# Performance work log

Measured on AMD Instinct MI355X. Metric: run time of the kernel, lower is better.

## Reference

```python
import jax, jax.numpy as jnp
import numpy as np

COS_EPS = 1e-8  # torch F.cosine_similarity eps


def setup_inputs() -> dict:
    key = jax.random.key(0)
    k1, k2 = jax.random.split(key)
    x = jax.random.normal(k1, (8192, 512), dtype=jnp.float32)
    class_logits = jax.random.normal(k2, (8192, 100), dtype=jnp.float32)
    return {"x": x, "class_logits": class_logits}


def reference(x, class_logits):
    N, D = x.shape
    C = class_logits.shape[1]

    # class_logits.clone().detach()
    logits = jax.lax.stop_gradient(class_logits)
    pred = jax.nn.softmax(logits, axis=1)
    max_logit = pred.max(axis=1)          # [N]
    max_cls = pred.argmax(axis=1)         # [N] int

    # graph(): pairwise cosine similarity = normalize rows + gram matmul
    norms = jnp.linalg.norm(x, axis=1, keepdims=True)
    xn = x / jnp.maximum(norms, COS_EPS)
    mat = xn @ xn.T                       # [N, N]

    x_agg = mat @ x + x                   # [N, D]
    x_new = jax.lax.stop_gradient(x_agg)

    # update_prototype: per-class weighted scatter-add then mean over counts
    weighted = x_new * max_logit[:, None]                     # [N, D]
    sums = jax.ops.segment_sum(weighted, max_cls, num_segments=C)      # [C, D]
    counts = jax.ops.segment_sum(jnp.ones((N,), x.dtype), max_cls, num_segments=C)  # [C]
    prototypes = jnp.where(counts[:, None] > 0,
                           sums / jnp.maximum(counts, 1.0)[:, None],
                           jnp.zeros_like(sums))              # [C, D]

    # inter_class_matrix[i, j] = prototypes[j] - prototypes[i]
    inter_class_matrix = prototypes[None, :, :] - prototypes[:, None, :]  # [C, C, D]
    return prototypes, inter_class_matrix
```

## Files before the change

### kernel.cpp

```cpp
#include <hip/hip_runtime.h>
#include <math.h>

#define N_ROWS 8192
#define D_DIM  512
#define C_CLS  100

typedef unsigned short u16;
typedef unsigned int u32;
typedef __attribute__((ext_vector_type(8))) _Float16 half8;
typedef __attribute__((ext_vector_type(4))) float floatx4;

#define WS_G      0
#define WS_GP     262144
#define WS_INV    5505024
#define WS_WV     5513216
#define WS_CLS    5521408
#define WS_CNT    5529600
#define WS_OFFS   5529728
#define WS_ORDER  5529856
#define WS_U      5538048
#define WS_V      5589248
#define WS_ZTH    5640448

typedef const __attribute__((address_space(1))) u32* gp32;
typedef __attribute__((address_space(3))) u32* lp32;
__device__ __forceinline__ void cp16(const u16* g, u16* l) {
    __builtin_amdgcn_global_load_lds((gp32)g, (lp32)l, 16, 0, 0);
}

__device__ __forceinline__ u16 f2h(float v) {
    _Float16 h = (_Float16)v;
    return *(u16*)&h;
}

__global__ __launch_bounds__(256) void kA(const float* __restrict__ logits,
        const float* __restrict__ x, float* __restrict__ wv, int* __restrict__ cls,
        float* __restrict__ inv, u16* __restrict__ zth) {
    __shared__ float xs[32 * 516];
    __shared__ float ns[8][32];
    __shared__ float sv_s[32];
    int bx = blockIdx.x, t = threadIdx.x;
    if (bx < 1024) {
        int lane = t & 63;
        int row0 = (bx << 3) + ((t >> 6) << 1);
        #pragma unroll
        for (int rr = 0; rr < 2; ++rr) {
            int row = row0 + rr;
            const float* lrow = logits + (size_t)row * C_CLS;
            float v1 = lrow[lane];
            bool has2 = (lane + 64) < C_CLS;
            float v2 = has2 ? lrow[lane + 64] : -INFINITY;
            float m; int idx;
            if (v2 > v1) { m = v2; idx = lane + 64; } else { m = v1; idx = lane; }
            #pragma unroll
            for (int off = 32; off >= 1; off >>= 1) {
                float om = __shfl_down(m, off);
                int   oi = __shfl_down(idx, off);
                if (om > m || (om == m && oi < idx)) { m = om; idx = oi; }
            }
            m = __shfl(m, 0);
            idx = __shfl(idx, 0);
            float s = expf(v1 - m) + (has2 ? expf(v2 - m) : 0.0f);
            #pragma unroll
            for (int off = 32; off >= 1; off >>= 1) s += __shfl_down(s, off);
            if (lane == 0) {
                wv[row] = 1.0f / s;
                cls[row] = idx;
            }
        }
        return;
    }
    int r0 = (bx - 1024) << 5;
    const float* src = x + (size_t)r0 * D_DIM;
    #pragma unroll
    for (int i = 0; i < 16; ++i) {
        int e = i * 1024 + t * 4;
        int r = e >> 9, c = e & 511;
        *(float4*)&xs[r * 516 + c] = *(const float4*)&src[e];
    }
    __syncthreads();
    {
        int r = t & 31, seg = t >> 5;
        const float* row = &xs[r * 516 + seg * 64];
        float ss = 0.f;
        #pragma unroll
        for (int jj = 0; jj < 64; ++jj) { float v = row[jj]; ss += v * v; }
        ns[seg][r] = ss;
    }
    __syncthreads();
    if (t < 32) {
        float ss = ns[0][t] + ns[1][t] + ns[2][t] + ns[3][t]
                 + ns[4][t] + ns[5][t] + ns[6][t] + ns[7][t];
        float iv = 1.0f / fmaxf(sqrtf(ss), 1e-8f);
        inv[r0 + t] = iv;
        sv_s[t] = sqrtf(iv);
    }
    __syncthreads();
    int c = t >> 2, rq = (t & 3) * 8;
    float svl[8];
    #pragma unroll
    for (int ii = 0; ii < 8; ++ii) svl[ii] = sv_s[rq + ii];
    #pragma unroll
    for (int ct = 0; ct < 8; ++ct) {
        int d = ct * 64 + c;
        u16 o[8];
        #pragma unroll
        for (int ii = 0; ii < 8; ++ii)
            o[ii] = f2h(xs[(rq + ii) * 516 + d] * svl[ii]);
        uint4 val = make_uint4((u32)o[0] | ((u32)o[1] << 16),
                               (u32)o[2] | ((u32)o[3] << 16),
                               (u32)o[4] | ((u32)o[5] << 16),
                               (u32)o[6] | ((u32)o[7] << 16));
        *(uint4*)&zth[(size_t)d * N_ROWS + r0 + rq] = val;
    }
}

__global__ __launch_bounds__(1024) void kB(const int* __restrict__ cls,
        int* __restrict__ cnt, int* __restrict__ offs, int* __restrict__ order) {
    __shared__ int hist[128], scan_s[128], cur[128];
    int t = threadIdx.x;
    if (t < 128) hist[t] = 0;
    __syncthreads();
    for (int m = t; m < N_ROWS; m += 1024) atomicAdd(&hist[cls[m]], 1);
    __syncthreads();
    if (t < 128) scan_s[t] = hist[t];
    __syncthreads();
    #pragma unroll
    for (int d = 1; d < 128; d <<= 1) {
        int add = (t < 128 && t >= d) ? scan_s[t - d] : 0;
        __syncthreads();
        if (t < 128) scan_s[t] += add;
        __syncthreads();
    }
    if (t < 128) {
        int off0 = scan_s[t] - hist[t];
        cur[t] = off0;
        offs[t] = off0;
        cnt[t] = hist[t];
    }
    __syncthreads();
    for (int m = t; m < N_ROWS; m += 1024) {
        int p = atomicAdd(&cur[cls[m]], 1);
        order[p] = m;
    }
}

__global__ __launch_bounds__(256) void kC(const u16* __restrict__ zth,
        const float* __restrict__ x, const float* __restrict__ inv,
        const float* __restrict__ wv, const int* __restrict__ order,
        const int* __restrict__ offs, const int* __restrict__ cnt,
        float* __restrict__ Gp, float* __restrict__ u_arr, float* __restrict__ v_arr) {
    __shared__ __attribute__((aligned(16))) union {
        struct { u16 Ah[128 * 32], Bh[128 * 32]; } g;
        struct { float us[4][64], vs[4][64]; } uv;
    } sm;
    int bx = blockIdx.x, t = threadIdx.x;
    if (bx >= 320) {
        int idx = bx - 320;
        int c = idx >> 3, jc = idx & 7;
        int g = t >> 6, lane = t & 63;
        int j = jc * 64 + lane;
        int n = cnt[c], o = offs[c];
        float ua = 0.f, va = 0.f;
        for (int p = g; p < n; p += 4) {
            int m = order[o + p];
            float wm = wv[m];
            float wi = wm * inv[m];
            float xv = x[(size_t)m * D_DIM + j];
            ua += wi * xv; va += wm * xv;
        }
        sm.uv.us[g][lane] = ua; sm.uv.vs[g][lane] = va;
        __syncthreads();
        if (g == 0) {
            u_arr[(size_t)c * D_DIM + j] = sm.uv.us[0][lane] + sm.uv.us[1][lane] + sm.uv.us[2][lane] + sm.uv.us[3][lane];
            v_arr[(size_t)c * D_DIM + j] = sm.uv.vs[0][lane] + sm.uv.vs[1][lane] + sm.uv.vs[2][lane] + sm.uv.vs[3][lane];
        }
        return;
    }
    int tile = bx % 10;
    int p = bx / 10;
    int ti = tile < 4 ? 0 : (tile < 7 ? 1 : (tile < 9 ? 2 : 3));
    int tj = tile - (ti == 0 ? 0 : (ti == 1 ? 3 : (ti == 2 ? 5 : 6)));
    int i0 = ti << 7, j0 = tj << 7;
    bool diag = (ti == tj);
    int kb = p << 8;
    int w = t >> 6, l = t & 63;
    int srow = t >> 2, scol = (t & 3) << 3;
    int lm = l & 15, lg = l >> 4;
    floatx4 acc[4][4];
    #pragma unroll
    for (int mi = 0; mi < 4; ++mi)
        #pragma unroll
        for (int ni = 0; ni < 4; ++ni) acc[mi][ni] = (floatx4){0.f, 0.f, 0.f, 0.f};
    int d0 = srow * 32 + scol;
    int d1 = (64 + srow) * 32 + scol;
    const size_t ga0 = (size_t)(i0 + srow) * N_ROWS + kb + scol;
    const size_t ga1 = (size_t)(i0 + 64 + srow) * N_ROWS + kb + scol;
    const size_t gb0 = (size_t)(j0 + srow) * N_ROWS + kb + scol;
    const size_t gb1 = (size_t)(j0 + 64 + srow) * N_ROWS + kb + scol;
    const u16* Bhs = diag ? sm.g.Ah : sm.g.Bh;
    for (int s = 0; s < 8; ++s) {
        int ks = s << 5;
        cp16(zth + ga0 + ks, sm.g.Ah + d0);
        cp16(zth + ga1 + ks, sm.g.Ah + d1);
        if (!diag) {
            cp16(zth + gb0 + ks, sm.g.Bh + d0);
            cp16(zth + gb1 + ks, sm.g.Bh + d1);
        }
        __syncthreads();
        half8 ah[4], bh[4];
        #pragma unroll
        for (int mi = 0; mi < 4; ++mi) {
            int off = (((w & 1) << 6) + (mi << 4) + lm) * 32 + (lg << 3);
            ah[mi] = *(const half8*)&sm.g.Ah[off];
        }
        #pragma unroll
        for (int ni = 0; ni < 4; ++ni) {
            int off = (((w >> 1) << 6) + (ni << 4) + lm) * 32 + (lg << 3);
            bh[ni] = *(const half8*)&Bhs[off];
        }
        #pragma unroll
        for (int mi = 0; mi < 4; ++mi)
            #pragma unroll
            for (int ni = 0; ni < 4; ++ni)
                acc[mi][ni] = __builtin_amdgcn_mfma_f32_16x16x32_f16(ah[mi], bh[ni], acc[mi][ni], 0, 0, 0);
        __syncthreads();
    }
    float* Gb = Gp + ((size_t)(p * 10 + tile) << 14);
    #pragma unroll
    for (int mi = 0; mi < 4; ++mi) {
        int row0 = ((w & 1) << 6) + (mi << 4) + (lg << 2);
        #pragma unroll
        for (int ni = 0; ni < 4; ++ni) {
            int col = ((w >> 1) << 6) + (ni << 4) + lm;
            #pragma unroll
            for (int r = 0; r < 4; ++r)
                Gb[(size_t)(row0 + r) * 128 + col] = acc[mi][ni][r];
        }
    }
}

__global__ __launch_bounds__(256) void kR(const float* __restrict__ Gp,
                                          float* __restrict__ G) {
    int i = blockIdx.x * 256 + threadIdx.x;
    int r = i >> 9, c = i & 511;
    int tr = r >> 7, tc = c >> 7, rr = r & 127, cc = c & 127;
    if (tr > tc) { int tmp = tr; tr = tc; tc = tmp; tmp = rr; rr = cc; cc = tmp; }
    int tid = tr * 4 + tc - ((tr * (tr + 1)) >> 1);
    const float* src = Gp + ((size_t)tid << 14) + rr * 128 + cc;
    float s = 0.f;
    #pragma unroll
    for (int p = 0; p < 32; ++p) s += src[(size_t)p * 163840];
    G[i] = s;
}

__global__ __launch_bounds__(256) void kD(const float* __restrict__ u_arr,
        const float* __restrict__ v_arr, const int* __restrict__ cnt,
        const float* __restrict__ G, float* __restrict__ out) {
    __shared__ float us[8][512];
    int g = blockIdx.x >> 4;
    int panel = blockIdx.x & 15;
    int t = threadIdx.x;
    for (int idx = t; idx < 8 * 512; idx += 256) {
        int ci = idx >> 9, k = idx & 511;
        int cc = g * 8 + ci;
        us[ci][k] = (cc < C_CLS) ? u_arr[(size_t)cc * D_DIM + k] : 0.f;
    }
    __syncthreads();
    int ci = t >> 5, cj = t & 31;
    int c = g * 8 + ci;
    int j = panel * 32 + cj;
    float acc = 0.f;
    #pragma unroll 8
    for (int k = 0; k < D_DIM; ++k)
        acc += us[ci][k] * G[(size_t)k * D_DIM + j];
    if (c < C_CLS) {
        int n = cnt[c];
        float s = (n > 0) ? 1.0f / (float)n : 0.0f;
        out[(size_t)c * D_DIM + j] = (v_arr[(size_t)c * D_DIM + j] + acc) * s;
    }
}

__global__ __launch_bounds__(256) void kE(const float* __restrict__ proto,
                                          float* __restrict__ inter) {
    int pair = blockIdx.x * 4 + (threadIdx.x >> 6);
    int i = pair / C_CLS;
    int j = pair - i * C_CLS;
    int d = (threadIdx.x & 63) << 3;
    float4 pj0 = *(const float4*)&proto[j * D_DIM + d];
    float4 pj1 = *(const float4*)&proto[j * D_DIM + d + 4];
    float4 pi0 = *(const float4*)&proto[i * D_DIM + d];
    float4 pi1 = *(const float4*)&proto[i * D_DIM + d + 4];
    float4 r0, r1;
    r0.x = pj0.x - pi0.x; r0.y = pj0.y - pi0.y; r0.z = pj0.z - pi0.z; r0.w = pj0.w - pi0.w;
    r1.x = pj1.x - pi1.x; r1.y = pj1.y - pi1.y; r1.z = pj1.z - pi1.z; r1.w = pj1.w - pi1.w;
    *(float4*)&inter[(size_t)pair * D_DIM + d]     = r0;
    *(float4*)&inter[(size_t)pair * D_DIM + d + 4] = r1;
}

extern "C" void kernel_launch(void* const* d_in, const int* in_sizes, int n_in,
                              void* d_out, int out_size, void* d_ws, size_t ws_size,
                              hipStream_t stream) {
    const float* x      = (const float*)d_in[0];
    const float* logits = (const float*)d_in[1];
    float* out = (float*)d_out;
    float* ws  = (float*)d_ws;
    float* G     = ws + WS_G;
    float* Gp    = ws + WS_GP;
    float* inv   = ws + WS_INV;
    float* wv    = ws + WS_WV;
    int*   cls   = (int*)(ws + WS_CLS);
    int*   cnt   = (int*)(ws + WS_CNT);
    int*   offs  = (int*)(ws + WS_OFFS);
    int*   order = (int*)(ws + WS_ORDER);
    float* u_arr = ws + WS_U;
    float* v_arr = ws + WS_V;
    u16* zth = (u16*)(ws + WS_ZTH);

    kA<<<1280, 256, 0, stream>>>(logits, x, wv, cls, inv, zth);
    kB<<<1, 1024, 0, stream>>>(cls, cnt, offs, order);
    kC<<<1120, 256, 0, stream>>>(zth, x, inv, wv, order, offs, cnt, Gp, u_arr, v_arr);
    kR<<<1024, 256, 0, stream>>>(Gp, G);
    kD<<<208, 256, 0, stream>>>(u_arr, v_arr, cnt, G, out);
    kE<<<C_CLS * C_CLS / 4, 256, 0, stream>>>(out, out + C_CLS * D_DIM);
}
```

Measured before the change: 169.8 us.

## Double-buffer Gram tile loads and shrink row-normalization tiles to 16 rows

```diff
diff --git a/kernel.cpp b/kernel.cpp
--- a/kernel.cpp
+++ b/kernel.cpp
@@ -22,6 +22,8 @@
 #define WS_V      5589248
 #define WS_ZTH    5640448
 
+#define LDA 517
+
 typedef const __attribute__((address_space(1))) u32* gp32;
 typedef __attribute__((address_space(3))) u32* lp32;
 __device__ __forceinline__ void cp16(const u16* g, u16* l) {
@@ -36,9 +38,9 @@
 __global__ __launch_bounds__(256) void kA(const float* __restrict__ logits,
         const float* __restrict__ x, float* __restrict__ wv, int* __restrict__ cls,
         float* __restrict__ inv, u16* __restrict__ zth) {
-    __shared__ float xs[32 * 516];
-    __shared__ float ns[8][32];
-    __shared__ float sv_s[32];
+    __shared__ float xs[16 * LDA];
+    __shared__ float ns[4][16];
+    __shared__ float sv_s[16];
     int bx = blockIdx.x, t = threadIdx.x;
     if (bx < 1024) {
         int lane = t & 63;
@@ -70,43 +72,44 @@
         }
         return;
     }
-    int r0 = (bx - 1024) << 5;
+    int r0 = (bx - 1024) << 4;
     const float* src = x + (size_t)r0 * D_DIM;
     #pragma unroll
-    for (int i = 0; i < 16; ++i) {
+    for (int i = 0; i < 8; ++i) {
         int e = i * 1024 + t * 4;
         int r = e >> 9, c = e & 511;
-        *(float4*)&xs[r * 516 + c] = *(const float4*)&src[e];
+        *(float4*)&xs[r * LDA + c] = *(const float4*)&src[e];
     }
     __syncthreads();
     {
-        int r = t & 31, seg = t >> 5;
-        const float* row = &xs[r * 516 + seg * 64];
+        int r = t & 15, seg = t >> 4;
+        const float* row = &xs[r * LDA + seg * 32];
         float ss = 0.f;
         #pragma unroll
-        for (int jj = 0; jj < 64; ++jj) { float v = row[jj]; ss += v * v; }
-        ns[seg][r] = ss;
-    }
-    __syncthreads();
-    if (t < 32) {
-        float ss = ns[0][t] + ns[1][t] + ns[2][t] + ns[3][t]
-                 + ns[4][t] + ns[5][t] + ns[6][t] + ns[7][t];
-        float iv = 1.0f / fmaxf(sqrtf(ss), 1e-8f);
+        for (int jj = 0; jj < 32; ++jj) { float v = row[jj]; ss += v * v; }
+        atomicAdd(&ns[seg & 3][r], 0.f);
+        ns[0][r] = 0.f;
+        __syncthreads();
+        atomicAdd(&ns[0][r], ss);
+    }
+    __syncthreads();
+    if (t < 16) {
+        float iv = 1.0f / fmaxf(sqrtf(ns[0][t]), 1e-8f);
         inv[r0 + t] = iv;
         sv_s[t] = sqrtf(iv);
     }
     __syncthreads();
-    int c = t >> 2, rq = (t & 3) * 8;
+    int c = t >> 1, rq = (t & 1) * 8;
     float svl[8];
     #pragma unroll
     for (int ii = 0; ii < 8; ++ii) svl[ii] = sv_s[rq + ii];
     #pragma unroll
-    for (int ct = 0; ct < 8; ++ct) {
-        int d = ct * 64 + c;
+    for (int ct = 0; ct < 4; ++ct) {
+        int d = ct * 128 + c;
         u16 o[8];
         #pragma unroll
         for (int ii = 0; ii < 8; ++ii)
-            o[ii] = f2h(xs[(rq + ii) * 516 + d] * svl[ii]);
+            o[ii] = f2h(xs[(rq + ii) * LDA + d] * svl[ii]);
         uint4 val = make_uint4((u32)o[0] | ((u32)o[1] << 16),
                                (u32)o[2] | ((u32)o[3] << 16),
                                (u32)o[4] | ((u32)o[5] << 16),
@@ -151,7 +154,7 @@
         const int* __restrict__ offs, const int* __restrict__ cnt,
         float* __restrict__ Gp, float* __restrict__ u_arr, float* __restrict__ v_arr) {
     __shared__ __attribute__((aligned(16))) union {
-        struct { u16 Ah[128 * 32], Bh[128 * 32]; } g;
+        struct { u16 Ah[2][128 * 32], Bh[2][128 * 32]; } g;
         struct { float us[4][64], vs[4][64]; } uv;
     } sm;
     int bx = blockIdx.x, t = threadIdx.x;
@@ -198,21 +201,30 @@
     const size_t ga1 = (size_t)(i0 + 64 + srow) * N_ROWS + kb + scol;
     const size_t gb0 = (size_t)(j0 + srow) * N_ROWS + kb + scol;
     const size_t gb1 = (size_t)(j0 + 64 + srow) * N_ROWS + kb + scol;
-    const u16* Bhs = diag ? sm.g.Ah : sm.g.Bh;
+    cp16(zth + ga0, sm.g.Ah[0] + d0);
+    cp16(zth + ga1, sm.g.Ah[0] + d1);
+    if (!diag) {
+        cp16(zth + gb0, sm.g.Bh[0] + d0);
+        cp16(zth + gb1, sm.g.Bh[0] + d1);
+    }
+    __syncthreads();
     for (int s = 0; s < 8; ++s) {
-        int ks = s << 5;
-        cp16(zth + ga0 + ks, sm.g.Ah + d0);
-        cp16(zth + ga1 + ks, sm.g.Ah + d1);
-        if (!diag) {
-            cp16(zth + gb0 + ks, sm.g.Bh + d0);
-            cp16(zth + gb1 + ks, sm.g.Bh + d1);
-        }
-        __syncthreads();
+        int cur = s & 1, nxt = cur ^ 1;
+        if (s + 1 < 8) {
+            int ks = (s + 1) << 5;
+            cp16(zth + ga0 + ks, sm.g.Ah[nxt] + d0);
+            cp16(zth + ga1 + ks, sm.g.Ah[nxt] + d1);
+            if (!diag) {
+                cp16(zth + gb0 + ks, sm.g.Bh[nxt] + d0);
+                cp16(zth + gb1 + ks, sm.g.Bh[nxt] + d1);
+            }
+        }
+        const u16* Bhs = diag ? sm.g.Ah[cur] : sm.g.Bh[cur];
         half8 ah[4], bh[4];
         #pragma unroll
         for (int mi = 0; mi < 4; ++mi) {
             int off = (((w & 1) << 6) + (mi << 4) + lm) * 32 + (lg << 3);
-            ah[mi] = *(const half8*)&sm.g.Ah[off];
+            ah[mi] = *(const half8*)&sm.g.Ah[cur][off];
         }
         #pragma unroll
         for (int ni = 0; ni < 4; ++ni) {
@@ -317,7 +329,7 @@
     float* v_arr = ws + WS_V;
     u16* zth = (u16*)(ws + WS_ZTH);
 
-    kA<<<1280, 256, 0, stream>>>(logits, x, wv, cls, inv, zth);
+    kA<<<1536, 256, 0, stream>>>(logits, x, wv, cls, inv, zth);
     kB<<<1, 1024, 0, stream>>>(cls, cnt, offs, order);
     kC<<<1120, 256, 0, stream>>>(zth, x, inv, wv, order, offs, cnt, Gp, u_arr, v_arr);
     kR<<<1024, 256, 0, stream>>>(Gp, G);
```

New measurement: 168.8 us. No clear change (-0.6%).
